# Kernel optimization log

Measured on AMD Instinct MI355X. Metric: run time of the kernel, lower is better.

## Reference

```python
import jax, jax.numpy as jnp
import numpy as np

SLOPE = 25.0   # fast_sigmoid surrogate slope
THR = 1.0      # snntorch Leaky default threshold


@jax.custom_vjp
def spike(x):
    # Heaviside forward, fast-sigmoid surrogate backward
    return (x > 0).astype(x.dtype)

def _spike_fwd(x):
    return spike(x), x

def _spike_bwd(x, g):
    return (g / (SLOPE * jnp.abs(x) + 1.0) ** 2,)

spike.defvjp(_spike_fwd, _spike_bwd)


def conv2d(x, w, b):
    y = jax.lax.conv_general_dilated(
        x, w, window_strides=(1, 1), padding=((1, 1), (1, 1)),
        dimension_numbers=('NCHW', 'OIHW', 'NCHW'))
    return y + b[None, :, None, None]


def maxpool2(x):
    return jax.lax.reduce_window(x, -jnp.inf, jax.lax.max,
                                 (1, 1, 2, 2), (1, 1, 2, 2), 'VALID')


def bn_inf(x, g, b, m, v):
    # inference-mode BatchNorm2d, eps = 1e-5
    inv = g * jax.lax.rsqrt(v + 1e-5)
    return x * inv[None, :, None, None] + (b - m * inv)[None, :, None, None]


def lif_step(mem, inp, beta):
    # snntorch Leaky, reset_mechanism='subtract', learn_beta (clamped to [0,1])
    b = jnp.clip(beta, 0.0, 1.0)
    reset = jax.lax.stop_gradient((mem > THR).astype(mem.dtype))
    mem_new = b * mem + inp - reset * THR
    spk = spike(mem_new - THR)
    return spk, mem_new


def setup_inputs() -> dict:
    key = jax.random.key(0)
    ks = jax.random.split(key, 20)
    T, B, H, W = 25, 512, 100, 64   # T steps, batch, MAX_LEN, N_MELS
    NUM_CLASSES = 35
    FLAT = 32 * (H // 4) * (W // 4)  # 12800
    f32 = jnp.float32
    inp = {
        'x': jax.random.normal(ks[0], (T, B, H, W), f32),
        'conv1_w': jax.random.normal(ks[1], (16, 1, 3, 3), f32) * 0.2,
        'conv1_b': jnp.zeros((16,), f32),
        'bn1_g': jnp.ones((16,), f32),
        'bn1_b': jnp.zeros((16,), f32),
        'bn1_m': jax.random.normal(ks[2], (16,), f32) * 0.1,
        'bn1_v': jax.random.uniform(ks[3], (16,), f32) + 0.5,
        'conv2_w': jax.random.normal(ks[4], (32, 16, 3, 3), f32) * (1.0 / np.sqrt(16 * 9)),
        'conv2_b': jnp.zeros((32,), f32),
        'bn2_g': jnp.ones((32,), f32),
        'bn2_b': jnp.zeros((32,), f32),
        'bn2_m': jax.random.normal(ks[5], (32,), f32) * 0.1,
        'bn2_v': jax.random.uniform(ks[6], (32,), f32) + 0.5,
        'fc1_w': jax.random.normal(ks[7], (256, FLAT), f32) * (1.0 / np.sqrt(FLAT)),
        'fc1_b': jnp.zeros((256,), f32),
        'fc2_w': jax.random.normal(ks[8], (128, 256), f32) * (1.0 / np.sqrt(256)),
        'fc2_b': jnp.zeros((128,), f32),
        'fc3_w': jax.random.normal(ks[9], (NUM_CLASSES, 128), f32) * (1.0 / np.sqrt(128)),
        'fc3_b': jnp.zeros((NUM_CLASSES,), f32),
        'beta1': jnp.float32(0.9),
        'beta2': jnp.float32(0.9),
        'beta3': jnp.float32(0.9),
    }
    return inp


def reference(x, conv1_w, conv1_b, bn1_g, bn1_b, bn1_m, bn1_v,
              conv2_w, conv2_b, bn2_g, bn2_b, bn2_m, bn2_v,
              fc1_w, fc1_b, fc2_w, fc2_b, fc3_w, fc3_b,
              beta1, beta2, beta3):
    T, B = x.shape[0], x.shape[1]
    # CNN runs once on the time-averaged input
    x_mean = jnp.mean(x, axis=0)[:, None]          # (B, 1, H, W)
    f = maxpool2(jax.nn.relu(bn_inf(conv2d(x_mean, conv1_w, conv1_b), bn1_g, bn1_b, bn1_m, bn1_v)))
    f = maxpool2(jax.nn.relu(bn_inf(conv2d(f, conv2_w, conv2_b), bn2_g, bn2_b, bn2_m, bn2_v)))
    feat = f.reshape(B, -1)                        # (B, FLAT)
    # fc1 input is the same every step (dropout = identity in eval)
    cur1 = feat @ fc1_w.T + fc1_b                  # (B, 256)

    m1 = jnp.zeros((B, fc1_w.shape[0]), x.dtype)
    m2 = jnp.zeros((B, fc2_w.shape[0]), x.dtype)
    m3 = jnp.zeros((B, fc3_w.shape[0]), x.dtype)

    def step(carry, _):
        m1, m2, m3 = carry
        spk1, m1 = lif_step(m1, cur1, beta1)
        spk2, m2 = lif_step(m2, spk1 @ fc2_w.T + fc2_b, beta2)
        spk3, m3 = lif_step(m3, spk2 @ fc3_w.T + fc3_b, beta3)
        return (m1, m2, m3), spk3

    _, out = jax.lax.scan(step, (m1, m2, m3), None, length=T)
    return out                                     # (T, B, NUM_CLASSES)
```

## Files before the change

kernel.cpp:

```cpp
#include <hip/hip_runtime.h>

#define N_P1    (512*16*50*32)
#define N_FEAT  (512*12800)
#define N_PART  (32*512*256)

#define WS_P1    0
#define WS_FEAT  (WS_P1 + N_P1)
#define WS_PART  (WS_FEAT + N_FEAT)

__global__ __launch_bounds__(256) void conv1_kernel(const float* __restrict__ x,
                                                    const float* __restrict__ w1,
                                                    const float* __restrict__ cb1,
                                                    const float* __restrict__ g1,
                                                    const float* __restrict__ bb1,
                                                    const float* __restrict__ m1g,
                                                    const float* __restrict__ v1,
                                                    float* __restrict__ p1) {
    __shared__ float xs[22 * 66];
    __shared__ float w1s[144];
    __shared__ float sh1s[16];
    const int b = blockIdx.x, s = blockIdx.y;
    const int tid = threadIdx.x;
    if (tid < 144) {
        int c = tid / 9;
        float inv = g1[c] * rsqrtf(v1[c] + 1e-5f);
        w1s[tid] = w1[tid] * inv;
    }
    if (tid < 16) {
        float inv = g1[tid] * rsqrtf(v1[tid] + 1e-5f);
        sh1s[tid] = cb1[tid] * inv + bb1[tid] - m1g[tid] * inv;
    }
    if (tid < 44) xs[(tid >> 1) * 66 + (tid & 1) * 65] = 0.f;
    const int r0 = s * 20 - 1;
    const size_t TSTR = (size_t)512 * 6400;
    for (int i = tid; i < 22 * 16; i += 256) {
        int lr = i >> 4, cq = i & 15;
        int gr = r0 + lr;
        float4 a0 = make_float4(0.f, 0.f, 0.f, 0.f), a1 = a0, a2 = a0, a3 = a0;
        if (gr >= 0 && gr < 100) {
            const float* px = x + (size_t)b * 6400 + gr * 64 + cq * 4;
            #pragma unroll
            for (int tt = 0; tt < 24; tt += 4) {
                float4 v0 = *(const float4*)(px + (size_t)(tt + 0) * TSTR);
                float4 v1_ = *(const float4*)(px + (size_t)(tt + 1) * TSTR);
                float4 v2_ = *(const float4*)(px + (size_t)(tt + 2) * TSTR);
                float4 v3 = *(const float4*)(px + (size_t)(tt + 3) * TSTR);
                a0.x += v0.x; a0.y += v0.y; a0.z += v0.z; a0.w += v0.w;
                a1.x += v1_.x; a1.y += v1_.y; a1.z += v1_.z; a1.w += v1_.w;
                a2.x += v2_.x; a2.y += v2_.y; a2.z += v2_.z; a2.w += v2_.w;
                a3.x += v3.x; a3.y += v3.y; a3.z += v3.z; a3.w += v3.w;
            }
            float4 v = *(const float4*)(px + (size_t)24 * TSTR);
            a0.x += v.x; a0.y += v.y; a0.z += v.z; a0.w += v.w;
        }
        const float sc = 1.0f / 25.0f;
        float* d = &xs[lr * 66 + 1 + cq * 4];
        d[0] = (a0.x + a1.x + a2.x + a3.x) * sc;
        d[1] = (a0.y + a1.y + a2.y + a3.y) * sc;
        d[2] = (a0.z + a1.z + a2.z + a3.z) * sc;
        d[3] = (a0.w + a1.w + a2.w + a3.w) * sc;
    }
    __syncthreads();
    for (int pos = tid; pos < 320; pos += 256) {
        int phl = pos >> 5, pw = pos & 31;
        int ph = s * 10 + phl;
        float win[4][4];
        #pragma unroll
        for (int a = 0; a < 4; ++a)
            #pragma unroll
            for (int c2 = 0; c2 < 4; ++c2)
                win[a][c2] = xs[(2 * phl + a) * 66 + 2 * pw + c2];
        #pragma unroll 1
        for (int c = 0; c < 16; ++c) {
            float s00 = 0.f, s01 = 0.f, s10 = 0.f, s11 = 0.f;
            #pragma unroll
            for (int dh = 0; dh < 3; ++dh)
                #pragma unroll
                for (int dw = 0; dw < 3; ++dw) {
                    float w = w1s[c * 9 + dh * 3 + dw];
                    s00 = fmaf(win[dh][dw],         w, s00);
                    s01 = fmaf(win[dh][dw + 1],     w, s01);
                    s10 = fmaf(win[dh + 1][dw],     w, s10);
                    s11 = fmaf(win[dh + 1][dw + 1], w, s11);
                }
            float m = fmaxf(fmaxf(s00, s01), fmaxf(s10, s11));
            float val = fmaxf(m + sh1s[c], 0.f);
            p1[(((size_t)b * 16 + c) * 50 + ph) * 32 + pw] = val;
        }
    }
}

__global__ __launch_bounds__(256) void conv2_kernel(const float* __restrict__ p1,
                                                    const float* __restrict__ w2g,
                                                    const float* __restrict__ cb2,
                                                    const float* __restrict__ g2,
                                                    const float* __restrict__ bb2,
                                                    const float* __restrict__ m2g,
                                                    const float* __restrict__ v2,
                                                    float* __restrict__ feat) {
    __shared__ float ins[16 * 18 * 36];
    __shared__ float wl[16 * 9 * 32];
    __shared__ float sh2s[32];
    const int bid = blockIdx.x;
    const int b = bid >> 2, s = bid & 3;
    const int tid = threadIdx.x;
    const int chg = tid & 15, phl = (tid >> 4) & 7, half = tid >> 7;
    const int ph = s * 8 + phl;

    for (int i = tid; i < 288; i += 256) {
        int ci = i / 18, lr = i - ci * 18;
        int gr = s * 16 - 1 + lr;
        float* dst = &ins[(ci * 18 + lr) * 36];
        if (gr >= 0 && gr < 50) {
            const float* src = p1 + (((size_t)b * 16 + ci) * 50 + gr) * 32;
            float4 v0 = *(const float4*)src;
            dst[0] = 0.f; dst[1] = v0.x; dst[2] = v0.y; dst[3] = v0.z;
            #pragma unroll
            for (int q = 1; q < 8; ++q) {
                float4 v = *(const float4*)(src + 4 * q - 1);
                *(float4*)(dst + 4 * q) = v;
            }
            dst[32] = src[31];
            dst[33] = 0.f; dst[34] = 0.f; dst[35] = 0.f;
        } else {
            #pragma unroll
            for (int q = 0; q < 9; ++q) *(float4*)(dst + 4 * q) = make_float4(0.f, 0.f, 0.f, 0.f);
        }
    }
    for (int i = tid; i < 4608; i += 256) {
        int c = i / 144, rem = i - c * 144;
        float inv = g2[c] * rsqrtf(v2[c] + 1e-5f);
        wl[rem * 32 + c] = w2g[i] * inv;
    }
    if (tid < 32) {
        float inv = g2[tid] * rsqrtf(v2[tid] + 1e-5f);
        sh2s[tid] = cb2[tid] * inv + bb2[tid] - m2g[tid] * inv;
    }
    __syncthreads();

    if (ph < 25) {
        float acc[2][2][16];
        #pragma unroll
        for (int a = 0; a < 2; ++a)
            #pragma unroll
            for (int r = 0; r < 2; ++r)
                #pragma unroll
                for (int xx = 0; xx < 16; ++xx) acc[a][r][xx] = 0.f;
        const int xb = half * 16;
        #pragma unroll 1
        for (int ci = 0; ci < 16; ++ci) {
            float2 wv[9];
            #pragma unroll
            for (int t = 0; t < 9; ++t)
                wv[t] = *(const float2*)&wl[(ci * 9 + t) * 32 + 2 * chg];
            #pragma unroll
            for (int lr4 = 0; lr4 < 4; ++lr4) {
                const float* row = &ins[(ci * 18 + (2 * phl + lr4)) * 36 + xb];
                float v[18];
                float4 t0 = *(const float4*)&row[0];
                float4 t1 = *(const float4*)&row[4];
                float4 t2 = *(const float4*)&row[8];
                float4 t3 = *(const float4*)&row[12];
                v[0]=t0.x; v[1]=t0.y; v[2]=t0.z; v[3]=t0.w;
                v[4]=t1.x; v[5]=t1.y; v[6]=t1.z; v[7]=t1.w;
                v[8]=t2.x; v[9]=t2.y; v[10]=t2.z; v[11]=t2.w;
                v[12]=t3.x; v[13]=t3.y; v[14]=t3.z; v[15]=t3.w;
                v[16] = row[16]; v[17] = row[17];
                #pragma unroll
                for (int a = 0; a < 2; ++a) {
                    const int dh = lr4 - a;
                    if (dh >= 0 && dh <= 2) {
                        #pragma unroll
                        for (int dw = 0; dw < 3; ++dw) {
                            float w0 = wv[dh * 3 + dw].x;
                            float w1 = wv[dh * 3 + dw].y;
                            #pragma unroll
                            for (int xx = 0; xx < 16; ++xx) {
                                acc[0][a][xx] = fmaf(v[xx + dw], w0, acc[0][a][xx]);
                                acc[1][a][xx] = fmaf(v[xx + dw], w1, acc[1][a][xx]);
                            }
                        }
                    }
                }
            }
        }
        #pragma unroll
        for (int ch = 0; ch < 2; ++ch) {
            const int c = 2 * chg + ch;
            const float sh = sh2s[c];
            #pragma unroll
            for (int pwl = 0; pwl < 8; ++pwl) {
                float m = fmaxf(fmaxf(acc[ch][0][2 * pwl], acc[ch][0][2 * pwl + 1]),
                                fmaxf(acc[ch][1][2 * pwl], acc[ch][1][2 * pwl + 1]));
                float val = fmaxf(m + sh, 0.f);
                feat[(((size_t)b * 32 + c) * 25 + ph) * 16 + half * 8 + pwl] = val;
            }
        }
    }
}

__global__ __launch_bounds__(256) void fc1_kernel(const float* __restrict__ feat,
                                                  const float* __restrict__ w,
                                                  float* __restrict__ part) {
    __shared__ float As[16 * 136];
    __shared__ float Bs[16 * 136];
    const int bx = blockIdx.x, by = blockIdx.y, bz = blockIdx.z;
    const int tid = threadIdx.x;
    const int tm = tid >> 4, tn = tid & 15;
    const int r = tid >> 2, cq = tid & 3;
    const int m0 = bx * 128, n0 = by * 128;
    const size_t aBase = (size_t)(m0 + r) * 12800 + bz * 400 + cq * 4;
    const size_t bBase = (size_t)(n0 + r) * 12800 + bz * 400 + cq * 4;
    float acc[8][8];
    #pragma unroll
    for (int i = 0; i < 8; ++i)
        #pragma unroll
        for (int j = 0; j < 8; ++j) acc[i][j] = 0.f;

    for (int kt = 0; kt < 25; ++kt) {
        float4 a0 = *(const float4*)(feat + aBase + kt * 16);
        float4 a1 = *(const float4*)(feat + aBase + (size_t)64 * 12800 + kt * 16);
        float4 b0 = *(const float4*)(w    + bBase + kt * 16);
        float4 b1 = *(const float4*)(w    + bBase + (size_t)64 * 12800 + kt * 16);
        __syncthreads();
        As[(cq * 4 + 0) * 136 + r]      = a0.x; As[(cq * 4 + 1) * 136 + r]      = a0.y;
        As[(cq * 4 + 2) * 136 + r]      = a0.z; As[(cq * 4 + 3) * 136 + r]      = a0.w;
        As[(cq * 4 + 0) * 136 + 64 + r] = a1.x; As[(cq * 4 + 1) * 136 + 64 + r] = a1.y;
        As[(cq * 4 + 2) * 136 + 64 + r] = a1.z; As[(cq * 4 + 3) * 136 + 64 + r] = a1.w;
        Bs[(cq * 4 + 0) * 136 + r]      = b0.x; Bs[(cq * 4 + 1) * 136 + r]      = b0.y;
        Bs[(cq * 4 + 2) * 136 + r]      = b0.z; Bs[(cq * 4 + 3) * 136 + r]      = b0.w;
        Bs[(cq * 4 + 0) * 136 + 64 + r] = b1.x; Bs[(cq * 4 + 1) * 136 + 64 + r] = b1.y;
        Bs[(cq * 4 + 2) * 136 + 64 + r] = b1.z; Bs[(cq * 4 + 3) * 136 + 64 + r] = b1.w;
        __syncthreads();
        #pragma unroll
        for (int kk = 0; kk < 16; ++kk) {
            float4 av0 = *(const float4*)&As[kk * 136 + tm * 8];
            float4 av1 = *(const float4*)&As[kk * 136 + tm * 8 + 4];
            float4 bv0 = *(const float4*)&Bs[kk * 136 + tn * 8];
            float4 bv1 = *(const float4*)&Bs[kk * 136 + tn * 8 + 4];
            float a_[8] = {av0.x, av0.y, av0.z, av0.w, av1.x, av1.y, av1.z, av1.w};
            float b_[8] = {bv0.x, bv0.y, bv0.z, bv0.w, bv1.x, bv1.y, bv1.z, bv1.w};
            #pragma unroll
            for (int i = 0; i < 8; ++i)
                #pragma unroll
                for (int j = 0; j < 8; ++j)
                    acc[i][j] = fmaf(a_[i], b_[j], acc[i][j]);
        }
    }
    #pragma unroll
    for (int i = 0; i < 8; ++i) {
        float* dst = &part[(size_t)bz * 131072 + (size_t)(m0 + tm * 8 + i) * 256 + n0 + tn * 8];
        *(float4*)dst       = make_float4(acc[i][0], acc[i][1], acc[i][2], acc[i][3]);
        *(float4*)(dst + 4) = make_float4(acc[i][4], acc[i][5], acc[i][6], acc[i][7]);
    }
}

__global__ __launch_bounds__(128) void scan_kernel(const float* __restrict__ part,
                                                   const float* __restrict__ b1g,
                                                   const float* __restrict__ w2g,
                                                   const float* __restrict__ b2g,
                                                   const float* __restrict__ w3g,
                                                   const float* __restrict__ b3g,
                                                   const float* __restrict__ pb1,
                                                   const float* __restrict__ pb2,
                                                   const float* __restrict__ pb3,
                                                   float* __restrict__ out) {
    __shared__ float  w2T[256 * 128];
    __shared__ float  w3T[128 * 36];
    __shared__ float  spkT[2][256];
    __shared__ float  spk2T[2][128];
    __shared__ float4 red[64];
    __shared__ float2 red3[64];
    const int tid = threadIdx.x;
    const int wv = tid >> 6, lane = tid & 63;
    const int b0 = blockIdx.x * 2;
    const int myrow = wv;
    for (int i = tid; i < 8192; i += 128) {
        int j = i >> 6, k4 = i & 63;
        float4 v = *(const float4*)&w2g[j * 256 + k4 * 4];
        w2T[(k4 * 4 + 0) * 128 + j] = v.x; w2T[(k4 * 4 + 1) * 128 + j] = v.y;
        w2T[(k4 * 4 + 2) * 128 + j] = v.z; w2T[(k4 * 4 + 3) * 128 + j] = v.w;
    }
    for (int i = tid; i < 4480; i += 128) { int j = i >> 7, k = i & 127; w3T[k * 36 + j] = w3g[i]; }
    float cu[4];
    {
        float4 s = *(const float4*)&b1g[lane * 4];
        const float* p = part + (size_t)(b0 + myrow) * 256 + lane * 4;
        #pragma unroll 8
        for (int z = 0; z < 32; ++z) {
            float4 v = *(const float4*)(p + (size_t)z * 131072);
            s.x += v.x; s.y += v.y; s.z += v.z; s.w += v.w;
        }
        cu[0] = s.x; cu[1] = s.y; cu[2] = s.z; cu[3] = s.w;
    }
    __syncthreads();
    const float be1 = fminf(fmaxf(pb1[0], 0.f), 1.f);
    const float be2 = fminf(fmaxf(pb2[0], 0.f), 1.f);
    const float be3 = fminf(fmaxf(pb3[0], 0.f), 1.f);
    float2 bias2 = *(const float2*)&b2g[lane * 2];
    float bias3 = (lane < 35) ? b3g[lane] : 0.f;
    float m1[4] = {0.f, 0.f, 0.f, 0.f};
    float m2[2][2] = {{0.f, 0.f}, {0.f, 0.f}};
    float m3[2] = {0.f, 0.f};
    const int kbase = wv * 128;

    for (int t = 0; t < 25; ++t) {
        float4 s1;
        {
            float r0 = (m1[0] > 1.f) ? 1.f : 0.f;
            float r1 = (m1[1] > 1.f) ? 1.f : 0.f;
            float r2 = (m1[2] > 1.f) ? 1.f : 0.f;
            float r3 = (m1[3] > 1.f) ? 1.f : 0.f;
            m1[0] = fmaf(be1, m1[0], cu[0]) - r0;
            m1[1] = fmaf(be1, m1[1], cu[1]) - r1;
            m1[2] = fmaf(be1, m1[2], cu[2]) - r2;
            m1[3] = fmaf(be1, m1[3], cu[3]) - r3;
            s1.x = (m1[0] > 1.f) ? 1.f : 0.f;
            s1.y = (m1[1] > 1.f) ? 1.f : 0.f;
            s1.z = (m1[2] > 1.f) ? 1.f : 0.f;
            s1.w = (m1[3] > 1.f) ? 1.f : 0.f;
        }
        *(float4*)&spkT[myrow][lane * 4] = s1;
        __syncthreads();
        float a00 = 0.f, a01 = 0.f, a10 = 0.f, a11 = 0.f;
        #pragma unroll 8
        for (int k4 = 0; k4 < 32; ++k4) {
            float4 sr0 = *(const float4*)&spkT[0][kbase + k4 * 4];
            float4 sr1 = *(const float4*)&spkT[1][kbase + k4 * 4];
            const float* wp = &w2T[(kbase + k4 * 4) * 128 + 2 * lane];
            float2 w0 = *(const float2*)(wp);
            float2 w1 = *(const float2*)(wp + 128);
            float2 w2 = *(const float2*)(wp + 256);
            float2 w3 = *(const float2*)(wp + 384);
            a00 = fmaf(sr0.x, w0.x, a00); a01 = fmaf(sr0.x, w0.y, a01);
            a10 = fmaf(sr1.x, w0.x, a10); a11 = fmaf(sr1.x, w0.y, a11);
            a00 = fmaf(sr0.y, w1.x, a00); a01 = fmaf(sr0.y, w1.y, a01);
            a10 = fmaf(sr1.y, w1.x, a10); a11 = fmaf(sr1.y, w1.y, a11);
            a00 = fmaf(sr0.z, w2.x, a00); a01 = fmaf(sr0.z, w2.y, a01);
            a10 = fmaf(sr1.z, w2.x, a10); a11 = fmaf(sr1.z, w2.y, a11);
            a00 = fmaf(sr0.w, w3.x, a00); a01 = fmaf(sr0.w, w3.y, a01);
            a10 = fmaf(sr1.w, w3.x, a10); a11 = fmaf(sr1.w, w3.y, a11);
        }
        if (wv == 1) red[lane] = make_float4(a00, a01, a10, a11);
        __syncthreads();
        if (wv == 0) {
            float4 o = red[lane];
            float in00 = a00 + o.x + bias2.x, in01 = a01 + o.y + bias2.y;
            float in10 = a10 + o.z + bias2.x, in11 = a11 + o.w + bias2.y;
            float r00 = (m2[0][0] > 1.f) ? 1.f : 0.f;
            float r01 = (m2[0][1] > 1.f) ? 1.f : 0.f;
            float r10 = (m2[1][0] > 1.f) ? 1.f : 0.f;
            float r11 = (m2[1][1] > 1.f) ? 1.f : 0.f;
            m2[0][0] = fmaf(be2, m2[0][0], in00) - r00;
            m2[0][1] = fmaf(be2, m2[0][1], in01) - r01;
            m2[1][0] = fmaf(be2, m2[1][0], in10) - r10;
            m2[1][1] = fmaf(be2, m2[1][1], in11) - r11;
            float2 sa, sb;
            sa.x = (m2[0][0] > 1.f) ? 1.f : 0.f;
            sa.y = (m2[0][1] > 1.f) ? 1.f : 0.f;
            sb.x = (m2[1][0] > 1.f) ? 1.f : 0.f;
            sb.y = (m2[1][1] > 1.f) ? 1.f : 0.f;
            *(float2*)&spk2T[0][lane * 2] = sa;
            *(float2*)&spk2T[1][lane * 2] = sb;
        }
        __syncthreads();
        float a3r0 = 0.f, a3r1 = 0.f;
        if (lane < 35) {
            const int k3 = wv * 64;
            #pragma unroll 4
            for (int k4 = 0; k4 < 16; ++k4) {
                float4 q0 = *(const float4*)&spk2T[0][k3 + k4 * 4];
                float4 q1 = *(const float4*)&spk2T[1][k3 + k4 * 4];
                const float* wp = &w3T[(k3 + k4 * 4) * 36 + lane];
                float wa = wp[0], wb = wp[36], wc = wp[72], wd = wp[108];
                a3r0 = fmaf(q0.x, wa, a3r0); a3r1 = fmaf(q1.x, wa, a3r1);
                a3r0 = fmaf(q0.y, wb, a3r0); a3r1 = fmaf(q1.y, wb, a3r1);
                a3r0 = fmaf(q0.z, wc, a3r0); a3r1 = fmaf(q1.z, wc, a3r1);
                a3r0 = fmaf(q0.w, wd, a3r0); a3r1 = fmaf(q1.w, wd, a3r1);
            }
        }
        if (wv == 1) red3[lane] = make_float2(a3r0, a3r1);
        __syncthreads();
        if (wv == 0 && lane < 35) {
            float2 o = red3[lane];
            float in0 = a3r0 + o.x + bias3;
            float in1 = a3r1 + o.y + bias3;
            float r0 = (m3[0] > 1.f) ? 1.f : 0.f;
            float r1 = (m3[1] > 1.f) ? 1.f : 0.f;
            m3[0] = fmaf(be3, m3[0], in0) - r0;
            m3[1] = fmaf(be3, m3[1], in1) - r1;
            out[((size_t)t * 512 + b0 + 0) * 35 + lane] = (m3[0] > 1.f) ? 1.f : 0.f;
            out[((size_t)t * 512 + b0 + 1) * 35 + lane] = (m3[1] > 1.f) ? 1.f : 0.f;
        }
    }
}

extern "C" void kernel_launch(void* const* d_in, const int* in_sizes, int n_in,
                              void* d_out, int out_size, void* d_ws, size_t ws_size,
                              hipStream_t stream) {
    const float* x     = (const float*)d_in[0];
    const float* c1w   = (const float*)d_in[1];
    const float* c1b   = (const float*)d_in[2];
    const float* bn1g  = (const float*)d_in[3];
    const float* bn1b  = (const float*)d_in[4];
    const float* bn1m  = (const float*)d_in[5];
    const float* bn1v  = (const float*)d_in[6];
    const float* c2w   = (const float*)d_in[7];
    const float* c2b   = (const float*)d_in[8];
    const float* bn2g  = (const float*)d_in[9];
    const float* bn2b  = (const float*)d_in[10];
    const float* bn2m  = (const float*)d_in[11];
    const float* bn2v  = (const float*)d_in[12];
    const float* fc1w  = (const float*)d_in[13];
    const float* fc1b  = (const float*)d_in[14];
    const float* fc2w  = (const float*)d_in[15];
    const float* fc2b  = (const float*)d_in[16];
    const float* fc3w  = (const float*)d_in[17];
    const float* fc3b  = (const float*)d_in[18];
    const float* beta1 = (const float*)d_in[19];
    const float* beta2 = (const float*)d_in[20];
    const float* beta3 = (const float*)d_in[21];
    float* ws  = (float*)d_ws;
    float* out = (float*)d_out;

    conv1_kernel<<<dim3(512, 5), 256, 0, stream>>>(x, c1w, c1b, bn1g, bn1b, bn1m, bn1v,
                                                   ws + WS_P1);
    conv2_kernel<<<2048, 256, 0, stream>>>(ws + WS_P1, c2w, c2b, bn2g, bn2b, bn2m, bn2v,
                                           ws + WS_FEAT);
    fc1_kernel<<<dim3(4, 2, 32), 256, 0, stream>>>(ws + WS_FEAT, fc1w, ws + WS_PART);
    scan_kernel<<<256, 128, 0, stream>>>(ws + WS_PART, fc1b, fc2w, fc2b, fc3w, fc3b,
                                         beta1, beta2, beta3, out);
}
```

Baseline: 348.9 us.

## Split recurrent scan into batched LIF and GEMM kernels, retile conv2 and fc1

```diff
diff --git a/kernel.cpp b/kernel.cpp
--- a/kernel.cpp
+++ b/kernel.cpp
@@ -7,6 +7,9 @@
 #define WS_P1    0
 #define WS_FEAT  (WS_P1 + N_P1)
 #define WS_PART  (WS_FEAT + N_FEAT)
+#define WS_S1    0
+#define WS_IN2   3276800
+#define WS_S2    4915200
 
 __global__ __launch_bounds__(256) void conv1_kernel(const float* __restrict__ x,
                                                     const float* __restrict__ w1,
@@ -90,7 +93,7 @@
     }
 }
 
-__global__ __launch_bounds__(256) void conv2_kernel(const float* __restrict__ p1,
+__global__ __launch_bounds__(320) void conv2_kernel(const float* __restrict__ p1,
                                                     const float* __restrict__ w2g,
                                                     const float* __restrict__ cb2,
                                                     const float* __restrict__ g2,
@@ -98,36 +101,35 @@
                                                     const float* __restrict__ m2g,
                                                     const float* __restrict__ v2,
                                                     float* __restrict__ feat) {
-    __shared__ float ins[16 * 18 * 36];
+    __shared__ float ins[16 * 12 * 36];
     __shared__ float wl[16 * 9 * 32];
     __shared__ float sh2s[32];
-    const int bid = blockIdx.x;
-    const int b = bid >> 2, s = bid & 3;
+    const int b = blockIdx.x, s = blockIdx.y;
     const int tid = threadIdx.x;
-    const int chg = tid & 15, phl = (tid >> 4) & 7, half = tid >> 7;
-    const int ph = s * 8 + phl;
-
-    for (int i = tid; i < 288; i += 256) {
-        int ci = i / 18, lr = i - ci * 18;
-        int gr = s * 16 - 1 + lr;
-        float* dst = &ins[(ci * 18 + lr) * 36];
+    const int chg = tid & 15, q = (tid >> 4) & 3, phl = tid >> 6;
+    const int ph = s * 5 + phl;
+
+    for (int i = tid; i < 192; i += 320) {
+        int ci = i / 12, lr = i - ci * 12;
+        int gr = s * 10 - 1 + lr;
+        float* dst = &ins[(ci * 12 + lr) * 36];
         if (gr >= 0 && gr < 50) {
             const float* src = p1 + (((size_t)b * 16 + ci) * 50 + gr) * 32;
             float4 v0 = *(const float4*)src;
             dst[0] = 0.f; dst[1] = v0.x; dst[2] = v0.y; dst[3] = v0.z;
             #pragma unroll
-            for (int q = 1; q < 8; ++q) {
-                float4 v = *(const float4*)(src + 4 * q - 1);
-                *(float4*)(dst + 4 * q) = v;
+            for (int qq = 1; qq < 8; ++qq) {
+                float4 v = *(const float4*)(src + 4 * qq - 1);
+                *(float4*)(dst + 4 * qq) = v;
             }
             dst[32] = src[31];
             dst[33] = 0.f; dst[34] = 0.f; dst[35] = 0.f;
         } else {
             #pragma unroll
-            for (int q = 0; q < 9; ++q) *(float4*)(dst + 4 * q) = make_float4(0.f, 0.f, 0.f, 0.f);
-        }
-    }
-    for (int i = tid; i < 4608; i += 256) {
+            for (int qq = 0; qq < 9; ++qq) *(float4*)(dst + 4 * qq) = make_float4(0.f, 0.f, 0.f, 0.f);
+        }
+    }
+    for (int i = tid; i < 4608; i += 320) {
         int c = i / 144, rem = i - c * 144;
         float inv = g2[c] * rsqrtf(v2[c] + 1e-5f);
         wl[rem * 32 + c] = w2g[i] * inv;
@@ -138,63 +140,58 @@
     }
     __syncthreads();
 
-    if (ph < 25) {
-        float acc[2][2][16];
+    float acc[2][2][8];
+    #pragma unroll
+    for (int c = 0; c < 2; ++c)
         #pragma unroll
         for (int a = 0; a < 2; ++a)
             #pragma unroll
-            for (int r = 0; r < 2; ++r)
-                #pragma unroll
-                for (int xx = 0; xx < 16; ++xx) acc[a][r][xx] = 0.f;
-        const int xb = half * 16;
-        #pragma unroll 1
-        for (int ci = 0; ci < 16; ++ci) {
-            float2 wv[9];
-            #pragma unroll
-            for (int t = 0; t < 9; ++t)
-                wv[t] = *(const float2*)&wl[(ci * 9 + t) * 32 + 2 * chg];
-            #pragma unroll
-            for (int lr4 = 0; lr4 < 4; ++lr4) {
-                const float* row = &ins[(ci * 18 + (2 * phl + lr4)) * 36 + xb];
-                float v[18];
-                float4 t0 = *(const float4*)&row[0];
-                float4 t1 = *(const float4*)&row[4];
-                float4 t2 = *(const float4*)&row[8];
-                float4 t3 = *(const float4*)&row[12];
-                v[0]=t0.x; v[1]=t0.y; v[2]=t0.z; v[3]=t0.w;
-                v[4]=t1.x; v[5]=t1.y; v[6]=t1.z; v[7]=t1.w;
-                v[8]=t2.x; v[9]=t2.y; v[10]=t2.z; v[11]=t2.w;
-                v[12]=t3.x; v[13]=t3.y; v[14]=t3.z; v[15]=t3.w;
-                v[16] = row[16]; v[17] = row[17];
-                #pragma unroll
-                for (int a = 0; a < 2; ++a) {
-                    const int dh = lr4 - a;
-                    if (dh >= 0 && dh <= 2) {
+            for (int xx = 0; xx < 8; ++xx) acc[c][a][xx] = 0.f;
+    const int xb = q * 8;
+    #pragma unroll 1
+    for (int ci = 0; ci < 16; ++ci) {
+        float2 wv[9];
+        #pragma unroll
+        for (int t = 0; t < 9; ++t)
+            wv[t] = *(const float2*)&wl[(ci * 9 + t) * 32 + 2 * chg];
+        #pragma unroll
+        for (int lr4 = 0; lr4 < 4; ++lr4) {
+            const float* row = &ins[(ci * 12 + (2 * phl + lr4)) * 36 + xb];
+            float v[10];
+            float4 t0 = *(const float4*)&row[0];
+            float4 t1 = *(const float4*)&row[4];
+            float2 t2 = *(const float2*)&row[8];
+            v[0]=t0.x; v[1]=t0.y; v[2]=t0.z; v[3]=t0.w;
+            v[4]=t1.x; v[5]=t1.y; v[6]=t1.z; v[7]=t1.w;
+            v[8]=t2.x; v[9]=t2.y;
+            #pragma unroll
+            for (int a = 0; a < 2; ++a) {
+                const int dh = lr4 - a;
+                if (dh >= 0 && dh <= 2) {
+                    #pragma unroll
+                    for (int dw = 0; dw < 3; ++dw) {
+                        float w0 = wv[dh * 3 + dw].x;
+                        float w1 = wv[dh * 3 + dw].y;
                         #pragma unroll
-                        for (int dw = 0; dw < 3; ++dw) {
-                            float w0 = wv[dh * 3 + dw].x;
-                            float w1 = wv[dh * 3 + dw].y;
-                            #pragma unroll
-                            for (int xx = 0; xx < 16; ++xx) {
-                                acc[0][a][xx] = fmaf(v[xx + dw], w0, acc[0][a][xx]);
-                                acc[1][a][xx] = fmaf(v[xx + dw], w1, acc[1][a][xx]);
-                            }
+                        for (int xx = 0; xx < 8; ++xx) {
+                            acc[0][a][xx] = fmaf(v[xx + dw], w0, acc[0][a][xx]);
+                            acc[1][a][xx] = fmaf(v[xx + dw], w1, acc[1][a][xx]);
                         }
                     }
                 }
             }
         }
-        #pragma unroll
-        for (int ch = 0; ch < 2; ++ch) {
-            const int c = 2 * chg + ch;
-            const float sh = sh2s[c];
-            #pragma unroll
-            for (int pwl = 0; pwl < 8; ++pwl) {
-                float m = fmaxf(fmaxf(acc[ch][0][2 * pwl], acc[ch][0][2 * pwl + 1]),
-                                fmaxf(acc[ch][1][2 * pwl], acc[ch][1][2 * pwl + 1]));
-                float val = fmaxf(m + sh, 0.f);
-                feat[(((size_t)b * 32 + c) * 25 + ph) * 16 + half * 8 + pwl] = val;
-            }
+    }
+    #pragma unroll
+    for (int ch = 0; ch < 2; ++ch) {
+        const int c = 2 * chg + ch;
+        const float sh = sh2s[c];
+        #pragma unroll
+        for (int p = 0; p < 4; ++p) {
+            float m = fmaxf(fmaxf(acc[ch][0][2 * p], acc[ch][0][2 * p + 1]),
+                            fmaxf(acc[ch][1][2 * p], acc[ch][1][2 * p + 1]));
+            float val = fmaxf(m + sh, 0.f);
+            feat[(((size_t)b * 32 + c) * 25 + ph) * 16 + q * 4 + p] = val;
         }
     }
 }
@@ -202,31 +199,28 @@
 __global__ __launch_bounds__(256) void fc1_kernel(const float* __restrict__ feat,
                                                   const float* __restrict__ w,
                                                   float* __restrict__ part) {
-    __shared__ float As[16 * 136];
+    __shared__ float As[16 * 68];
     __shared__ float Bs[16 * 136];
     const int bx = blockIdx.x, by = blockIdx.y, bz = blockIdx.z;
     const int tid = threadIdx.x;
     const int tm = tid >> 4, tn = tid & 15;
     const int r = tid >> 2, cq = tid & 3;
-    const int m0 = bx * 128, n0 = by * 128;
+    const int m0 = bx * 64, n0 = by * 128;
     const size_t aBase = (size_t)(m0 + r) * 12800 + bz * 400 + cq * 4;
     const size_t bBase = (size_t)(n0 + r) * 12800 + bz * 400 + cq * 4;
-    float acc[8][8];
-    #pragma unroll
-    for (int i = 0; i < 8; ++i)
+    float acc[4][8];
+    #pragma unroll
+    for (int i = 0; i < 4; ++i)
         #pragma unroll
         for (int j = 0; j < 8; ++j) acc[i][j] = 0.f;
 
     for (int kt = 0; kt < 25; ++kt) {
         float4 a0 = *(const float4*)(feat + aBase + kt * 16);
-        float4 a1 = *(const float4*)(feat + aBase + (size_t)64 * 12800 + kt * 16);
         float4 b0 = *(const float4*)(w    + bBase + kt * 16);
         float4 b1 = *(const float4*)(w    + bBase + (size_t)64 * 12800 + kt * 16);
         __syncthreads();
-        As[(cq * 4 + 0) * 136 + r]      = a0.x; As[(cq * 4 + 1) * 136 + r]      = a0.y;
-        As[(cq * 4 + 2) * 136 + r]      = a0.z; As[(cq * 4 + 3) * 136 + r]      = a0.w;
-        As[(cq * 4 + 0) * 136 + 64 + r] = a1.x; As[(cq * 4 + 1) * 136 + 64 + r] = a1.y;
-        As[(cq * 4 + 2) * 136 + 64 + r] = a1.z; As[(cq * 4 + 3) * 136 + 64 + r] = a1.w;
+        As[(cq * 4 + 0) * 68 + r] = a0.x; As[(cq * 4 + 1) * 68 + r] = a0.y;
+        As[(cq * 4 + 2) * 68 + r] = a0.z; As[(cq * 4 + 3) * 68 + r] = a0.w;
         Bs[(cq * 4 + 0) * 136 + r]      = b0.x; Bs[(cq * 4 + 1) * 136 + r]      = b0.y;
         Bs[(cq * 4 + 2) * 136 + r]      = b0.z; Bs[(cq * 4 + 3) * 136 + r]      = b0.w;
         Bs[(cq * 4 + 0) * 136 + 64 + r] = b1.x; Bs[(cq * 4 + 1) * 136 + 64 + r] = b1.y;
@@ -234,164 +228,150 @@
         __syncthreads();
         #pragma unroll
         for (int kk = 0; kk < 16; ++kk) {
-            float4 av0 = *(const float4*)&As[kk * 136 + tm * 8];
-            float4 av1 = *(const float4*)&As[kk * 136 + tm * 8 + 4];
+            float4 av  = *(const float4*)&As[kk * 68 + tm * 4];
             float4 bv0 = *(const float4*)&Bs[kk * 136 + tn * 8];
             float4 bv1 = *(const float4*)&Bs[kk * 136 + tn * 8 + 4];
-            float a_[8] = {av0.x, av0.y, av0.z, av0.w, av1.x, av1.y, av1.z, av1.w};
+            float a_[4] = {av.x, av.y, av.z, av.w};
             float b_[8] = {bv0.x, bv0.y, bv0.z, bv0.w, bv1.x, bv1.y, bv1.z, bv1.w};
             #pragma unroll
-            for (int i = 0; i < 8; ++i)
+            for (int i = 0; i < 4; ++i)
                 #pragma unroll
                 for (int j = 0; j < 8; ++j)
                     acc[i][j] = fmaf(a_[i], b_[j], acc[i][j]);
         }
     }
     #pragma unroll
-    for (int i = 0; i < 8; ++i) {
-        float* dst = &part[(size_t)bz * 131072 + (size_t)(m0 + tm * 8 + i) * 256 + n0 + tn * 8];
+    for (int i = 0; i < 4; ++i) {
+        float* dst = &part[(size_t)bz * 131072 + (size_t)(m0 + tm * 4 + i) * 256 + n0 + tn * 8];
         *(float4*)dst       = make_float4(acc[i][0], acc[i][1], acc[i][2], acc[i][3]);
         *(float4*)(dst + 4) = make_float4(acc[i][4], acc[i][5], acc[i][6], acc[i][7]);
     }
 }
 
-__global__ __launch_bounds__(128) void scan_kernel(const float* __restrict__ part,
+__global__ __launch_bounds__(256) void lif1_kernel(const float* __restrict__ part,
                                                    const float* __restrict__ b1g,
+                                                   const float* __restrict__ pb1,
+                                                   float* __restrict__ S1) {
+    const int i = blockIdx.x * 256 + threadIdx.x;
+    const int k = i & 255;
+    float cu = b1g[k];
+    #pragma unroll 8
+    for (int z = 0; z < 32; ++z) cu += part[(size_t)z * 131072 + i];
+    const float be = fminf(fmaxf(pb1[0], 0.f), 1.f);
+    float m = 0.f;
+    #pragma unroll
+    for (int t = 0; t < 25; ++t) {
+        float r = (m > 1.f) ? 1.f : 0.f;
+        m = fmaf(be, m, cu) - r;
+        S1[(size_t)t * 131072 + i] = (m > 1.f) ? 1.f : 0.f;
+    }
+}
+
+__global__ __launch_bounds__(256) void fc2g_kernel(const float* __restrict__ S1,
                                                    const float* __restrict__ w2g,
                                                    const float* __restrict__ b2g,
-                                                   const float* __restrict__ w3g,
-                                                   const float* __restrict__ b3g,
-                                                   const float* __restrict__ pb1,
+                                                   float* __restrict__ in2) {
+    __shared__ float As[16 * 36];
+    __shared__ float Bs[16 * 136];
+    const int m0 = blockIdx.x * 32;
+    const int tid = threadIdx.x;
+    const int tm = tid >> 4, tn = tid & 15;
+    float acc[2][8];
+    #pragma unroll
+    for (int i = 0; i < 2; ++i)
+        #pragma unroll
+        for (int j = 0; j < 8; ++j) acc[i][j] = 0.f;
+
+    for (int kt = 0; kt < 16; ++kt) {
+        float4 av = make_float4(0.f, 0.f, 0.f, 0.f);
+        if (tid < 128) {
+            int r = tid >> 2, cq = tid & 3;
+            av = *(const float4*)&S1[(size_t)(m0 + r) * 256 + kt * 16 + cq * 4];
+        }
+        int rb = tid >> 1, kb = (tid & 1) * 8;
+        float4 bv0 = *(const float4*)&w2g[rb * 256 + kt * 16 + kb];
+        float4 bv1 = *(const float4*)&w2g[rb * 256 + kt * 16 + kb + 4];
+        __syncthreads();
+        if (tid < 128) {
+            int r = tid >> 2, cq = tid & 3;
+            As[(cq * 4 + 0) * 36 + r] = av.x; As[(cq * 4 + 1) * 36 + r] = av.y;
+            As[(cq * 4 + 2) * 36 + r] = av.z; As[(cq * 4 + 3) * 36 + r] = av.w;
+        }
+        Bs[(kb + 0) * 136 + rb] = bv0.x; Bs[(kb + 1) * 136 + rb] = bv0.y;
+        Bs[(kb + 2) * 136 + rb] = bv0.z; Bs[(kb + 3) * 136 + rb] = bv0.w;
+        Bs[(kb + 4) * 136 + rb] = bv1.x; Bs[(kb + 5) * 136 + rb] = bv1.y;
+        Bs[(kb + 6) * 136 + rb] = bv1.z; Bs[(kb + 7) * 136 + rb] = bv1.w;
+        __syncthreads();
+        #pragma unroll
+        for (int kk = 0; kk < 16; ++kk) {
+            float2 a2 = *(const float2*)&As[kk * 36 + tm * 2];
+            float4 bv0_ = *(const float4*)&Bs[kk * 136 + tn * 8];
+            float4 bv1_ = *(const float4*)&Bs[kk * 136 + tn * 8 + 4];
+            float b_[8] = {bv0_.x, bv0_.y, bv0_.z, bv0_.w, bv1_.x, bv1_.y, bv1_.z, bv1_.w};
+            #pragma unroll
+            for (int j = 0; j < 8; ++j) {
+                acc[0][j] = fmaf(a2.x, b_[j], acc[0][j]);
+                acc[1][j] = fmaf(a2.y, b_[j], acc[1][j]);
+            }
+        }
+    }
+    float4 bb0 = *(const float4*)&b2g[tn * 8];
+    float4 bb1 = *(const float4*)&b2g[tn * 8 + 4];
+    #pragma unroll
+    for (int i = 0; i < 2; ++i) {
+        float* dst = &in2[(size_t)(m0 + tm * 2 + i) * 128 + tn * 8];
+        *(float4*)dst       = make_float4(acc[i][0] + bb0.x, acc[i][1] + bb0.y,
+                                          acc[i][2] + bb0.z, acc[i][3] + bb0.w);
+        *(float4*)(dst + 4) = make_float4(acc[i][4] + bb1.x, acc[i][5] + bb1.y,
+                                          acc[i][6] + bb1.z, acc[i][7] + bb1.w);
+    }
+}
+
+__global__ __launch_bounds__(256) void lif2_kernel(const float* __restrict__ in2,
                                                    const float* __restrict__ pb2,
-                                                   const float* __restrict__ pb3,
-                                                   float* __restrict__ out) {
-    __shared__ float  w2T[256 * 128];
-    __shared__ float  w3T[128 * 36];
-    __shared__ float  spkT[2][256];
-    __shared__ float  spk2T[2][128];
-    __shared__ float4 red[64];
-    __shared__ float2 red3[64];
-    const int tid = threadIdx.x;
-    const int wv = tid >> 6, lane = tid & 63;
-    const int b0 = blockIdx.x * 2;
-    const int myrow = wv;
-    for (int i = tid; i < 8192; i += 128) {
-        int j = i >> 6, k4 = i & 63;
-        float4 v = *(const float4*)&w2g[j * 256 + k4 * 4];
-        w2T[(k4 * 4 + 0) * 128 + j] = v.x; w2T[(k4 * 4 + 1) * 128 + j] = v.y;
-        w2T[(k4 * 4 + 2) * 128 + j] = v.z; w2T[(k4 * 4 + 3) * 128 + j] = v.w;
-    }
-    for (int i = tid; i < 4480; i += 128) { int j = i >> 7, k = i & 127; w3T[k * 36 + j] = w3g[i]; }
-    float cu[4];
-    {
-        float4 s = *(const float4*)&b1g[lane * 4];
-        const float* p = part + (size_t)(b0 + myrow) * 256 + lane * 4;
-        #pragma unroll 8
-        for (int z = 0; z < 32; ++z) {
-            float4 v = *(const float4*)(p + (size_t)z * 131072);
-            s.x += v.x; s.y += v.y; s.z += v.z; s.w += v.w;
-        }
-        cu[0] = s.x; cu[1] = s.y; cu[2] = s.z; cu[3] = s.w;
-    }
+                                                   float* __restrict__ S2) {
+    const int i = blockIdx.x * 256 + threadIdx.x;
+    const float be = fminf(fmaxf(pb2[0], 0.f), 1.f);
+    float m = 0.f;
+    #pragma unroll
+    for (int t = 0; t < 25; ++t) {
+        float r = (m > 1.f) ? 1.f : 0.f;
+        m = fmaf(be, m, in2[(size_t)t * 65536 + i]) - r;
+        S2[(size_t)t * 65536 + i] = (m > 1.f) ? 1.f : 0.f;
+    }
+}
+
+__global__ __launch_bounds__(64) void fc3l_kernel(const float* __restrict__ S2,
+                                                  const float* __restrict__ w3g,
+                                                  const float* __restrict__ b3g,
+                                                  const float* __restrict__ pb3,
+                                                  float* __restrict__ out) {
+    __shared__ float w3T[128 * 36];
+    __shared__ float s2row[128];
+    const int b = blockIdx.x;
+    const int lane = threadIdx.x;
+    for (int i = lane; i < 4480; i += 64) {
+        int j = i >> 7, k = i & 127;
+        w3T[k * 36 + j] = w3g[i];
+    }
+    const float be = fminf(fmaxf(pb3[0], 0.f), 1.f);
+    const float bias = (lane < 35) ? b3g[lane] : 0.f;
+    float m = 0.f;
     __syncthreads();
-    const float be1 = fminf(fmaxf(pb1[0], 0.f), 1.f);
-    const float be2 = fminf(fmaxf(pb2[0], 0.f), 1.f);
-    const float be3 = fminf(fmaxf(pb3[0], 0.f), 1.f);
-    float2 bias2 = *(const float2*)&b2g[lane * 2];
-    float bias3 = (lane < 35) ? b3g[lane] : 0.f;
-    float m1[4] = {0.f, 0.f, 0.f, 0.f};
-    float m2[2][2] = {{0.f, 0.f}, {0.f, 0.f}};
-    float m3[2] = {0.f, 0.f};
-    const int kbase = wv * 128;
-
     for (int t = 0; t < 25; ++t) {
-        float4 s1;
-        {
-            float r0 = (m1[0] > 1.f) ? 1.f : 0.f;
-            float r1 = (m1[1] > 1.f) ? 1.f : 0.f;
-            float r2 = (m1[2] > 1.f) ? 1.f : 0.f;
-            float r3 = (m1[3] > 1.f) ? 1.f : 0.f;
-            m1[0] = fmaf(be1, m1[0], cu[0]) - r0;
-            m1[1] = fmaf(be1, m1[1], cu[1]) - r1;
-            m1[2] = fmaf(be1, m1[2], cu[2]) - r2;
-            m1[3] = fmaf(be1, m1[3], cu[3]) - r3;
-            s1.x = (m1[0] > 1.f) ? 1.f : 0.f;
-            s1.y = (m1[1] > 1.f) ? 1.f : 0.f;
-            s1.z = (m1[2] > 1.f) ? 1.f : 0.f;
-            s1.w = (m1[3] > 1.f) ? 1.f : 0.f;
-        }
-        *(float4*)&spkT[myrow][lane * 4] = s1;
-        __syncthreads();
-        float a00 = 0.f, a01 = 0.f, a10 = 0.f, a11 = 0.f;
-        #pragma unroll 8
-        for (int k4 = 0; k4 < 32; ++k4) {
-            float4 sr0 = *(const float4*)&spkT[0][kbase + k4 * 4];
-            float4 sr1 = *(const float4*)&spkT[1][kbase + k4 * 4];
-            const float* wp = &w2T[(kbase + k4 * 4) * 128 + 2 * lane];
-            float2 w0 = *(const float2*)(wp);
-            float2 w1 = *(const float2*)(wp + 128);
-            float2 w2 = *(const float2*)(wp + 256);
-            float2 w3 = *(const float2*)(wp + 384);
-            a00 = fmaf(sr0.x, w0.x, a00); a01 = fmaf(sr0.x, w0.y, a01);
-            a10 = fmaf(sr1.x, w0.x, a10); a11 = fmaf(sr1.x, w0.y, a11);
-            a00 = fmaf(sr0.y, w1.x, a00); a01 = fmaf(sr0.y, w1.y, a01);
-            a10 = fmaf(sr1.y, w1.x, a10); a11 = fmaf(sr1.y, w1.y, a11);
-            a00 = fmaf(sr0.z, w2.x, a00); a01 = fmaf(sr0.z, w2.y, a01);
-            a10 = fmaf(sr1.z, w2.x, a10); a11 = fmaf(sr1.z, w2.y, a11);
-            a00 = fmaf(sr0.w, w3.x, a00); a01 = fmaf(sr0.w, w3.y, a01);
-            a10 = fmaf(sr1.w, w3.x, a10); a11 = fmaf(sr1.w, w3.y, a11);
-        }
-        if (wv == 1) red[lane] = make_float4(a00, a01, a10, a11);
-        __syncthreads();
-        if (wv == 0) {
-            float4 o = red[lane];
-            float in00 = a00 + o.x + bias2.x, in01 = a01 + o.y + bias2.y;
-            float in10 = a10 + o.z + bias2.x, in11 = a11 + o.w + bias2.y;
-            float r00 = (m2[0][0] > 1.f) ? 1.f : 0.f;
-            float r01 = (m2[0][1] > 1.f) ? 1.f : 0.f;
-            float r10 = (m2[1][0] > 1.f) ? 1.f : 0.f;
-            float r11 = (m2[1][1] > 1.f) ? 1.f : 0.f;
-            m2[0][0] = fmaf(be2, m2[0][0], in00) - r00;
-            m2[0][1] = fmaf(be2, m2[0][1], in01) - r01;
-            m2[1][0] = fmaf(be2, m2[1][0], in10) - r10;
-            m2[1][1] = fmaf(be2, m2[1][1], in11) - r11;
-            float2 sa, sb;
-            sa.x = (m2[0][0] > 1.f) ? 1.f : 0.f;
-            sa.y = (m2[0][1] > 1.f) ? 1.f : 0.f;
-            sb.x = (m2[1][0] > 1.f) ? 1.f : 0.f;
-            sb.y = (m2[1][1] > 1.f) ? 1.f : 0.f;
-            *(float2*)&spk2T[0][lane * 2] = sa;
-            *(float2*)&spk2T[1][lane * 2] = sb;
-        }
-        __syncthreads();
-        float a3r0 = 0.f, a3r1 = 0.f;
+        float2 v = *(const float2*)&S2[(size_t)t * 65536 + b * 128 + lane * 2];
+        *(float2*)&s2row[lane * 2] = v;
+        __syncthreads();
         if (lane < 35) {
-            const int k3 = wv * 64;
-            #pragma unroll 4
-            for (int k4 = 0; k4 < 16; ++k4) {
-                float4 q0 = *(const float4*)&spk2T[0][k3 + k4 * 4];
-                float4 q1 = *(const float4*)&spk2T[1][k3 + k4 * 4];
-                const float* wp = &w3T[(k3 + k4 * 4) * 36 + lane];
-                float wa = wp[0], wb = wp[36], wc = wp[72], wd = wp[108];
-                a3r0 = fmaf(q0.x, wa, a3r0); a3r1 = fmaf(q1.x, wa, a3r1);
-                a3r0 = fmaf(q0.y, wb, a3r0); a3r1 = fmaf(q1.y, wb, a3r1);
-                a3r0 = fmaf(q0.z, wc, a3r0); a3r1 = fmaf(q1.z, wc, a3r1);
-                a3r0 = fmaf(q0.w, wd, a3r0); a3r1 = fmaf(q1.w, wd, a3r1);
-            }
-        }
-        if (wv == 1) red3[lane] = make_float2(a3r0, a3r1);
-        __syncthreads();
-        if (wv == 0 && lane < 35) {
-            float2 o = red3[lane];
-            float in0 = a3r0 + o.x + bias3;
-            float in1 = a3r1 + o.y + bias3;
-            float r0 = (m3[0] > 1.f) ? 1.f : 0.f;
-            float r1 = (m3[1] > 1.f) ? 1.f : 0.f;
-            m3[0] = fmaf(be3, m3[0], in0) - r0;
-            m3[1] = fmaf(be3, m3[1], in1) - r1;
-            out[((size_t)t * 512 + b0 + 0) * 35 + lane] = (m3[0] > 1.f) ? 1.f : 0.f;
-            out[((size_t)t * 512 + b0 + 1) * 35 + lane] = (m3[1] > 1.f) ? 1.f : 0.f;
-        }
+            float a = bias;
+            #pragma unroll 8
+            for (int k = 0; k < 128; ++k)
+                a = fmaf(s2row[k], w3T[k * 36 + lane], a);
+            float r = (m > 1.f) ? 1.f : 0.f;
+            m = fmaf(be, m, a) - r;
+            out[((size_t)t * 512 + b) * 35 + lane] = (m > 1.f) ? 1.f : 0.f;
+        }
+        __syncthreads();
     }
 }
 
@@ -425,9 +405,11 @@
 
     conv1_kernel<<<dim3(512, 5), 256, 0, stream>>>(x, c1w, c1b, bn1g, bn1b, bn1m, bn1v,
                                                    ws + WS_P1);
-    conv2_kernel<<<2048, 256, 0, stream>>>(ws + WS_P1, c2w, c2b, bn2g, bn2b, bn2m, bn2v,
-                                           ws + WS_FEAT);
-    fc1_kernel<<<dim3(4, 2, 32), 256, 0, stream>>>(ws + WS_FEAT, fc1w, ws + WS_PART);
-    scan_kernel<<<256, 128, 0, stream>>>(ws + WS_PART, fc1b, fc2w, fc2b, fc3w, fc3b,
-                                         beta1, beta2, beta3, out);
-}
+    conv2_kernel<<<dim3(512, 5), 320, 0, stream>>>(ws + WS_P1, c2w, c2b, bn2g, bn2b, bn2m, bn2v,
+                                                   ws + WS_FEAT);
+    fc1_kernel<<<dim3(8, 2, 32), 256, 0, stream>>>(ws + WS_FEAT, fc1w, ws + WS_PART);
+    lif1_kernel<<<512, 256, 0, stream>>>(ws + WS_PART, fc1b, beta1, ws + WS_S1);
+    fc2g_kernel<<<400, 256, 0, stream>>>(ws + WS_S1, fc2w, fc2b, ws + WS_IN2);
+    lif2_kernel<<<256, 256, 0, stream>>>(ws + WS_IN2, beta2, ws + WS_S2);
+    fc3l_kernel<<<512, 64, 0, stream>>>(ws + WS_S2, fc3w, fc3b, beta3, out);
+}
```

Result: faster. 328.0 us (-6.0%).
